# Kernel tuning notes

Measured on AMD Instinct MI355X. Metric: run time of the kernel, lower is better.

The kernel has to match this reference:

```python
import jax, jax.numpy as jnp
from jax import lax
import numpy as np

CLASS_NUMBER = 19
REGION_RADIUS = 1
KERNEL = 2 * REGION_RADIUS + 1  # 3
IMAGE_TOPK = 256
EPS = 1e-6


def setup_inputs() -> dict:
    key = jax.random.key(0)
    # softmax-like probabilities over classes
    raw = jax.random.uniform(key, (4, CLASS_NUMBER, 512, 1024), dtype=jnp.float32)
    logit = raw / jnp.sum(raw, axis=1, keepdims=True)
    return {"logit": logit}


def _box_sum(x):
    # kxk box sum with zero padding (SAME for odd kernel == pad=radius)
    return lax.reduce_window(x, jnp.float32(0), lax.add,
                             (1, 1, KERNEL, KERNEL), (1, 1, 1, 1), 'SAME')


def reference(logit):
    B, C, H, W = logit.shape
    logC = jnp.log(jnp.float32(C))

    # region uncertainty: normalized entropy, then avg-pool (count_include_pad)
    entropy = jnp.sum(-logit * jnp.log(logit + EPS), axis=1, keepdims=True) / logC
    region_uncertainty = _box_sum(entropy) / (KERNEL * KERNEL)  # [B,1,H,W]

    # region impurity: argmax -> one-hot -> depthwise box-sum (ones kernel)
    predict = jnp.argmax(logit, axis=1)                       # [B,H,W]
    one_hot = jax.nn.one_hot(predict, C, axis=1, dtype=logit.dtype)  # [B,C,H,W]
    summary = _box_sum(one_hot)                               # [B,C,H,W]
    count = jnp.sum(summary, axis=1, keepdims=True)           # [B,1,H,W]
    dist = summary / count
    region_impurity = jnp.sum(-dist * jnp.log(dist + EPS), axis=1, keepdims=True) / logC

    score = region_uncertainty * region_impurity              # [B,1,H,W]

    # per-image score: sum of top-k region scores
    flat = score.reshape(B, H * W)
    topk_vals, _ = lax.top_k(flat, IMAGE_TOPK)
    image_score = jnp.sum(topk_vals, axis=1)                  # [B]
    return image_score
```

## Files before the change

kernel.cpp:

```cpp
#include <hip/hip_runtime.h>
#include <cstdint>
#include <cstddef>

#define BB 4
#define CC 19
#define HH 512
#define WW 1024
#define HW (HH*WW)
#define HW4 (HW/4)
#define BHW (BB*HW)
#define KTOP 256
#define EPSF 1e-6f
#define NB1 4096
#define NB2 8192
#define SEG 128
#define LSTRIDE 1032
#define LOGC 2.9444389791664403f

__device__ __forceinline__ unsigned int sortable(float x) {
    unsigned int u = __float_as_uint(x);
    return (u & 0x80000000u) ? ~u : (u | 0x80000000u);
}
__device__ __forceinline__ float unsortable(unsigned int K) {
    unsigned int u = (K & 0x80000000u) ? (K & 0x7FFFFFFFu) : ~K;
    return __uint_as_float(u);
}

__global__ __launch_bounds__(256) void k_ent(const float4* __restrict__ logit,
                                             float4* __restrict__ ent,
                                             uchar4* __restrict__ pred,
                                             unsigned int* __restrict__ histz,
                                             float* __restrict__ outz) {
    int idx = blockIdx.x * 256 + threadIdx.x;
    if (idx < 81928) histz[idx] = 0;
    if (idx < BB) outz[idx] = 0.f;
    int b = idx >> 17;
    int q = idx & (HW4 - 1);
    const float4* base = logit + (size_t)b * CC * HW4 + q;
    float e0 = 0.f, e1 = 0.f, e2 = 0.f, e3 = 0.f;
    float m0 = -1.f, m1 = -1.f, m2 = -1.f, m3 = -1.f;
    int a0 = 0, a1 = 0, a2 = 0, a3 = 0;
#pragma unroll
    for (int c = 0; c < CC; ++c) {
        float4 p = base[(size_t)c * HW4];
        e0 -= p.x * __logf(p.x + EPSF); if (p.x > m0) { m0 = p.x; a0 = c; }
        e1 -= p.y * __logf(p.y + EPSF); if (p.y > m1) { m1 = p.y; a1 = c; }
        e2 -= p.z * __logf(p.z + EPSF); if (p.z > m2) { m2 = p.z; a2 = c; }
        e3 -= p.w * __logf(p.w + EPSF); if (p.w > m3) { m3 = p.w; a3 = c; }
    }
    ent[idx] = make_float4(e0, e1, e2, e3);
    pred[idx] = make_uchar4((unsigned char)a0, (unsigned char)a1,
                            (unsigned char)a2, (unsigned char)a3);
}

__global__ __launch_bounds__(256) void k_score_hist(const float* __restrict__ ent,
                                                    const unsigned char* __restrict__ pred,
                                                    float* __restrict__ score,
                                                    unsigned int* __restrict__ hist1) {
    __shared__ __align__(16) float ent_s[6 * LSTRIDE];
    __shared__ __align__(16) unsigned char pred_s[6 * LSTRIDE];
    __shared__ unsigned int lh[NB1];
    __shared__ float lgt[48];
    int tid = threadIdx.x;
    int b = blockIdx.x >> 7;
    int seg = blockIdx.x & (SEG - 1);
    int r0 = seg * 4;

    for (int i = tid; i < 6 * LSTRIDE; i += 256) { ent_s[i] = 0.f; pred_s[i] = 255; }
    for (int i = tid; i < NB1; i += 256) lh[i] = 0;
    if (tid < 48) {
        int nvi = tid >> 4, cnt = tid & 15;
        float nv = (nvi == 0) ? 4.f : (nvi == 1) ? 6.f : 9.f;
        lgt[tid] = __logf((float)cnt / nv + EPSF);
    }
    __syncthreads();

    const float* eb = ent + (size_t)b * HW;
    const unsigned char* pb = pred + (size_t)b * HW;
    for (int i = tid; i < 1536; i += 256) {
        int rr = i >> 8, c4 = i & 255;
        int g = r0 - 1 + rr;
        if (g >= 0 && g < HH) {
            float4 v = *(const float4*)(eb + g * WW + c4 * 4);
            *(float4*)&ent_s[rr * LSTRIDE + 4 + c4 * 4] = v;
            uchar4 pv = *(const uchar4*)(pb + g * WW + c4 * 4);
            *(uchar4*)&pred_s[rr * LSTRIDE + 4 + c4 * 4] = pv;
        }
    }
    __syncthreads();

    float* sbuf = score + (size_t)b * HW;
#pragma unroll
    for (int it = 0; it < 16; ++it) {
        int p = it * 256 + tid;
        int py = p >> 10, px = p & 1023;
        int h = r0 + py, w = px;
        int l0 = py * LSTRIDE + 3 + px;
        float es = 0.f;
        int cls[9];
#pragma unroll
        for (int i = 0; i < 9; ++i) {
            int o = l0 + (i / 3) * LSTRIDE + (i % 3);
            es += ent_s[o];
            cls[i] = pred_s[o];
        }
        int nv = ((h > 0) + (h < HH - 1) + 1) * ((w > 0) + (w < WW - 1) + 1);
        float inv = 1.f / (float)nv;
        int nvi = (nv == 9) ? 2 : ((nv == 6) ? 1 : 0);
        const float* lg = &lgt[nvi * 16];
        float lsum = 0.f;
#pragma unroll
        for (int i = 0; i < 9; ++i) {
            int cnt = 0;
#pragma unroll
            for (int j = 0; j < 9; ++j) cnt += (cls[j] == cls[i]) ? 1 : 0;
            float lv = lg[cnt];
            lsum += (cls[i] != 255) ? lv : 0.f;
        }
        float imp = -inv * lsum;
        float v = (es * (1.f / (9.f * LOGC))) * (imp * (1.f / LOGC));
        sbuf[h * WW + w] = v;
        atomicAdd(&lh[sortable(v) >> 20], 1u);
    }
    __syncthreads();
    unsigned int* hb = hist1 + (size_t)b * NB1;
    for (int i = tid; i < NB1; i += 256) {
        unsigned int c = lh[i];
        if (c) atomicAdd(&hb[i], c);
    }
}

__device__ __forceinline__ void select4k(const unsigned int* __restrict__ hb,
                                         int rem, int* bin_out, int* rem_out) {
    __shared__ unsigned int cs[256];
    __shared__ unsigned int bs[16];
    __shared__ int s_chunk, s_bin, s_rem;
    int t = threadIdx.x;
    unsigned int s = 0;
#pragma unroll
    for (int i = 0; i < 16; ++i) s += hb[t * 16 + i];
    cs[t] = s;
    __syncthreads();
    for (int d = 1; d < 256; d <<= 1) {
        unsigned int v = (t + d < 256) ? cs[t + d] : 0;
        __syncthreads();
        cs[t] += v;
        __syncthreads();
    }
    unsigned int St = cs[t];
    unsigned int St1 = (t < 255) ? cs[t + 1] : 0;
    if ((int)St >= rem && (t == 255 || (int)St1 < rem)) {
        s_chunk = t; s_rem = rem - (int)St1;
    }
    __syncthreads();
    int chunk = s_chunk, rem2 = s_rem;
    if (t < 16) bs[t] = hb[chunk * 16 + t];
    __syncthreads();
    for (int d = 1; d < 16; d <<= 1) {
        unsigned int v = (t < 16 && t + d < 16) ? bs[t + d] : 0;
        __syncthreads();
        if (t < 16) bs[t] += v;
        __syncthreads();
    }
    if (t < 16) {
        unsigned int Sb = bs[t];
        unsigned int Sb1 = (t < 15) ? bs[t + 1] : 0;
        if ((int)Sb >= rem2 && (t == 15 || (int)Sb1 < rem2)) {
            s_bin = chunk * 16 + t; s_rem = rem2 - (int)Sb1;
        }
    }
    __syncthreads();
    *bin_out = s_bin;
    *rem_out = s_rem;
}

__device__ __forceinline__ void select8k(const unsigned int* __restrict__ hb,
                                         int rem, int* bin_out, int* rem_out) {
    __shared__ unsigned int cs[256];
    __shared__ unsigned int bs[32];
    __shared__ int s_chunk, s_bin, s_rem;
    int t = threadIdx.x;
    unsigned int s = 0;
#pragma unroll 8
    for (int i = 0; i < 32; ++i) s += hb[t * 32 + i];
    cs[t] = s;
    __syncthreads();
    for (int d = 1; d < 256; d <<= 1) {
        unsigned int v = (t + d < 256) ? cs[t + d] : 0;
        __syncthreads();
        cs[t] += v;
        __syncthreads();
    }
    unsigned int St = cs[t];
    unsigned int St1 = (t < 255) ? cs[t + 1] : 0;
    if ((int)St >= rem && (t == 255 || (int)St1 < rem)) {
        s_chunk = t; s_rem = rem - (int)St1;
    }
    __syncthreads();
    int chunk = s_chunk, rem2 = s_rem;
    if (t < 32) bs[t] = hb[chunk * 32 + t];
    __syncthreads();
    for (int d = 1; d < 32; d <<= 1) {
        unsigned int v = (t < 32 && t + d < 32) ? bs[t + d] : 0;
        __syncthreads();
        if (t < 32) bs[t] += v;
        __syncthreads();
    }
    if (t < 32) {
        unsigned int Sb = bs[t];
        unsigned int Sb1 = (t < 31) ? bs[t + 1] : 0;
        if ((int)Sb >= rem2 && (t == 31 || (int)Sb1 < rem2)) {
            s_bin = chunk * 32 + t; s_rem = rem2 - (int)Sb1;
        }
    }
    __syncthreads();
    *bin_out = s_bin;
    *rem_out = s_rem;
}

__global__ __launch_bounds__(256) void k_hist2(const float4* __restrict__ score,
                                               const unsigned int* __restrict__ hist1,
                                               unsigned int* __restrict__ hist2,
                                               float* __restrict__ hsum,
                                               unsigned int* __restrict__ T1g,
                                               int* __restrict__ r1g,
                                               float* __restrict__ out) {
    __shared__ unsigned int lh[NB2];
    __shared__ float ls[NB2];
    __shared__ float red[4];
    int b = blockIdx.x >> 7;
    int seg = blockIdx.x & (SEG - 1);
    int bin1, rem1;
    select4k(hist1 + (size_t)b * NB1, KTOP, &bin1, &rem1);
    unsigned int t1 = (unsigned int)bin1;
    if (seg == 0 && threadIdx.x == 0) { T1g[b] = t1; r1g[b] = rem1; }
    for (int i = threadIdx.x; i < NB2; i += 256) { lh[i] = 0; ls[i] = 0.f; }
    __syncthreads();
    const float4* p = score + ((size_t)b * HW + (size_t)seg * (HW / SEG)) / 4;
    float sa = 0.f;
    for (int i = threadIdx.x; i < (HW / SEG) / 4; i += 256) {
        float4 v = p[i];
        float vv[4] = {v.x, v.y, v.z, v.w};
#pragma unroll
        for (int q = 0; q < 4; ++q) {
            unsigned int k = sortable(vv[q]);
            unsigned int cb = k >> 20;
            if (cb > t1) sa += vv[q];
            else if (cb == t1) {
                int sub = (k >> 7) & 0x1FFF;
                atomicAdd(&lh[sub], 1u);
                atomicAdd(&ls[sub], vv[q]);
            }
        }
    }
    __syncthreads();
    unsigned int* hb = hist2 + (size_t)b * NB2;
    float* sb = hsum + (size_t)b * NB2;
    for (int i = threadIdx.x; i < NB2; i += 256) {
        unsigned int c = lh[i];
        if (c) { atomicAdd(&hb[i], c); atomicAdd(&sb[i], ls[i]); }
    }
#pragma unroll
    for (int d = 32; d; d >>= 1) sa += __shfl_down(sa, d);
    if ((threadIdx.x & 63) == 0) red[threadIdx.x >> 6] = sa;
    __syncthreads();
    if (threadIdx.x == 0) {
        float tt = red[0] + red[1] + red[2] + red[3];
        if (tt != 0.f) atomicAdd(&out[b], tt);
    }
}

__global__ __launch_bounds__(256) void k_scan2(const unsigned int* __restrict__ hist2,
                                               const float* __restrict__ hsum,
                                               const unsigned int* __restrict__ T1g,
                                               const int* __restrict__ r1g,
                                               float* __restrict__ out) {
    int b = blockIdx.x;
    int bin, rem;
    select8k(hist2 + (size_t)b * NB2, r1g[b], &bin, &rem);
    __shared__ float rs[256];
    int t = threadIdx.x;
    const float* sb = hsum + (size_t)b * NB2;
    float s = 0.f;
    for (int i = t; i < NB2; i += 256) if (i > bin) s += sb[i];
    rs[t] = s;
    __syncthreads();
    for (int d = 128; d; d >>= 1) {
        if (t < d) rs[t] += rs[t + d];
        __syncthreads();
    }
    if (t == 0) {
        unsigned int K = (T1g[b] << 20) | ((unsigned int)bin << 7);
        out[b] += rs[0] + unsortable(K) * (float)rem;
    }
}

extern "C" void kernel_launch(void* const* d_in, const int* in_sizes, int n_in,
                              void* d_out, int out_size, void* d_ws, size_t ws_size,
                              hipStream_t stream) {
    const float* logit = (const float*)d_in[0];
    float* out = (float*)d_out;
    char* ws = (char*)d_ws;

    float*         ent   = (float*)(ws);
    unsigned char* pred  = (unsigned char*)(ws + 8388608);
    float*         score = (float*)(ws + 10485760);
    unsigned int*  histb = (unsigned int*)(ws + 18874368);
    unsigned int*  hist1 = histb;
    unsigned int*  hist2 = histb + 16384;
    float*         hsum  = (float*)(histb + 49152);
    unsigned int*  T1g   = histb + 81920;
    int*           r1g   = (int*)(histb + 81924);

    k_ent<<<BHW / 4 / 256, 256, 0, stream>>>((const float4*)logit, (float4*)ent,
                                             (uchar4*)pred, histb, out);
    k_score_hist<<<BB * SEG, 256, 0, stream>>>(ent, pred, score, hist1);
    k_hist2<<<BB * SEG, 256, 0, stream>>>((const float4*)score, hist1,
                                          hist2, hsum, T1g, r1g, out);
    k_scan2<<<BB, 256, 0, stream>>>(hist2, hsum, T1g, r1g, out);
}
```

Baseline: 289.9 us.

## Fuse all stages into one cooperative persistent kernel with grid syncs

Replaces the four-kernel pipeline with a single cooperative kernel of 256 blocks. Each block computes entropy and argmax for 8 rows straight into shared memory and exchanges only the halo rows through global memory. Scores stay in registers for the second histogram pass, so the score buffer is never written or reread. The aim is to remove launch gaps and the intermediate ent, pred and score traffic. The cost is three grid-wide barriers, only 256 blocks of parallelism for the bandwidth-heavy logit read, and a fallback to the old path if the cooperative launch fails.

```diff
diff --git a/kernel.cpp b/kernel.cpp
--- a/kernel.cpp
+++ b/kernel.cpp
@@ -1,6 +1,9 @@
 #include <hip/hip_runtime.h>
+#include <hip/hip_cooperative_groups.h>
 #include <cstdint>
 #include <cstddef>
+
+namespace cg = cooperative_groups;
 
 #define BB 4
 #define CC 19
@@ -13,9 +16,12 @@
 #define EPSF 1e-6f
 #define NB1 4096
 #define NB2 8192
-#define SEG 128
 #define LSTRIDE 1032
 #define LOGC 2.9444389791664403f
+
+#define NSEG 64
+#define RPB 8
+#define SEGF 128
 
 __device__ __forceinline__ unsigned int sortable(float x) {
     unsigned int u = __float_as_uint(x);
@@ -24,6 +30,314 @@
 __device__ __forceinline__ float unsortable(unsigned int K) {
     unsigned int u = (K & 0x80000000u) ? (K & 0x7FFFFFFFu) : ~K;
     return __uint_as_float(u);
+}
+__device__ __forceinline__ unsigned int agld(const unsigned int* p) {
+    return __hip_atomic_load(p, __ATOMIC_RELAXED, __HIP_MEMORY_SCOPE_AGENT);
+}
+__device__ __forceinline__ void agst(unsigned int* p, unsigned int v) {
+    __hip_atomic_store(p, v, __ATOMIC_RELAXED, __HIP_MEMORY_SCOPE_AGENT);
+}
+
+struct P1Mem8 {
+    float ent_s[(RPB + 2) * LSTRIDE];
+    unsigned char pred_s[(RPB + 2) * LSTRIDE];
+    unsigned int lh1[NB1];
+};
+struct P2Mem8 {
+    unsigned int lh2[NB2];
+    float ls2[NB2];
+};
+union UMem8 { P1Mem8 p1; P2Mem8 p2; };
+
+__device__ __forceinline__ void sel_coarse(const unsigned int* __restrict__ hb,
+                                           int rem, unsigned int* cs, unsigned int* bs,
+                                           int* s3, int* bin_out, int* rem_out) {
+    int t = threadIdx.x;
+    unsigned int s = 0;
+#pragma unroll
+    for (int i = 0; i < 16; ++i) s += agld(&hb[t * 16 + i]);
+    cs[t] = s;
+    __syncthreads();
+    for (int d = 1; d < 256; d <<= 1) {
+        unsigned int v = (t + d < 256) ? cs[t + d] : 0;
+        __syncthreads();
+        cs[t] += v;
+        __syncthreads();
+    }
+    unsigned int St = cs[t];
+    unsigned int St1 = (t < 255) ? cs[t + 1] : 0;
+    if ((int)St >= rem && (t == 255 || (int)St1 < rem)) {
+        s3[0] = t; s3[2] = rem - (int)St1;
+    }
+    __syncthreads();
+    int chunk = s3[0], rem2 = s3[2];
+    if (t < 16) bs[t] = agld(&hb[chunk * 16 + t]);
+    __syncthreads();
+    for (int d = 1; d < 16; d <<= 1) {
+        unsigned int v = (t < 16 && t + d < 16) ? bs[t + d] : 0;
+        __syncthreads();
+        if (t < 16) bs[t] += v;
+        __syncthreads();
+    }
+    if (t < 16) {
+        unsigned int Sb = bs[t];
+        unsigned int Sb1 = (t < 15) ? bs[t + 1] : 0;
+        if ((int)Sb >= rem2 && (t == 15 || (int)Sb1 < rem2)) {
+            s3[1] = chunk * 16 + t; s3[2] = rem2 - (int)Sb1;
+        }
+    }
+    __syncthreads();
+    *bin_out = s3[1];
+    *rem_out = s3[2];
+}
+
+__device__ __forceinline__ void sel_fine(const unsigned int* __restrict__ hb,
+                                         int rem, unsigned int* cs, unsigned int* bs,
+                                         int* s3, int* bin_out, int* rem_out) {
+    int t = threadIdx.x;
+    unsigned int s = 0;
+#pragma unroll 8
+    for (int i = 0; i < 32; ++i) s += agld(&hb[t * 32 + i]);
+    cs[t] = s;
+    __syncthreads();
+    for (int d = 1; d < 256; d <<= 1) {
+        unsigned int v = (t + d < 256) ? cs[t + d] : 0;
+        __syncthreads();
+        cs[t] += v;
+        __syncthreads();
+    }
+    unsigned int St = cs[t];
+    unsigned int St1 = (t < 255) ? cs[t + 1] : 0;
+    if ((int)St >= rem && (t == 255 || (int)St1 < rem)) {
+        s3[0] = t; s3[2] = rem - (int)St1;
+    }
+    __syncthreads();
+    int chunk = s3[0], rem2 = s3[2];
+    if (t < 32) bs[t] = agld(&hb[chunk * 32 + t]);
+    __syncthreads();
+    for (int d = 1; d < 32; d <<= 1) {
+        unsigned int v = (t < 32 && t + d < 32) ? bs[t + d] : 0;
+        __syncthreads();
+        if (t < 32) bs[t] += v;
+        __syncthreads();
+    }
+    if (t < 32) {
+        unsigned int Sb = bs[t];
+        unsigned int Sb1 = (t < 31) ? bs[t + 1] : 0;
+        if ((int)Sb >= rem2 && (t == 31 || (int)Sb1 < rem2)) {
+            s3[1] = chunk * 32 + t; s3[2] = rem2 - (int)Sb1;
+        }
+    }
+    __syncthreads();
+    *bin_out = s3[1];
+    *rem_out = s3[2];
+}
+
+__global__ __launch_bounds__(256, 2) void k_fused8(const float* __restrict__ logit,
+                                                   float* __restrict__ ent,
+                                                   unsigned char* __restrict__ pred,
+                                                   unsigned int* __restrict__ histb,
+                                                   float* __restrict__ out) {
+    __shared__ __align__(16) UMem8 U;
+    __shared__ float lgt[48];
+    __shared__ unsigned int cs[256];
+    __shared__ unsigned int bs[32];
+    __shared__ int s3[3];
+    __shared__ float red[4];
+    __shared__ float rs[256];
+
+    cg::grid_group grid = cg::this_grid();
+    int tid = threadIdx.x;
+    int b = blockIdx.x >> 6;
+    int seg = blockIdx.x & (NSEG - 1);
+    int r0 = seg * RPB;
+
+    unsigned int* hist1 = histb;
+    unsigned int* hist2 = histb + 16384;
+    float*        hsum  = (float*)(histb + 49152);
+
+    int gid = blockIdx.x * 256 + tid;
+    for (int i = gid; i < 81920; i += 256 * 256) agst(&histb[i], 0u);
+    if (gid < BB) agst((unsigned int*)&out[gid], 0u);
+    if (tid < 48) {
+        int nvi = tid >> 4, cnt = tid & 15;
+        float nv = (nvi == 0) ? 4.f : (nvi == 1) ? 6.f : 9.f;
+        lgt[tid] = __logf((float)cnt / nv + EPSF);
+    }
+    for (int i = tid; i < (RPB + 2) * LSTRIDE; i += 256) { U.p1.ent_s[i] = 0.f; U.p1.pred_s[i] = 255; }
+    for (int i = tid; i < NB1; i += 256) U.p1.lh1[i] = 0;
+    __syncthreads();
+
+    {
+        const float4* bb4 = (const float4*)logit + (size_t)b * CC * HW4;
+        int q0 = r0 * 256;
+#pragma unroll
+        for (int it = 0; it < RPB; ++it) {
+            int q = q0 + it * 256 + tid;
+            const float4* basep = bb4 + q;
+            float e0 = 0.f, e1 = 0.f, e2 = 0.f, e3 = 0.f;
+            float m0 = -1.f, m1 = -1.f, m2 = -1.f, m3 = -1.f;
+            int a0 = 0, a1 = 0, a2 = 0, a3 = 0;
+#pragma unroll
+            for (int c = 0; c < CC; ++c) {
+                float4 p = basep[(size_t)c * HW4];
+                e0 -= p.x * __logf(p.x + EPSF); if (p.x > m0) { m0 = p.x; a0 = c; }
+                e1 -= p.y * __logf(p.y + EPSF); if (p.y > m1) { m1 = p.y; a1 = c; }
+                e2 -= p.z * __logf(p.z + EPSF); if (p.z > m2) { m2 = p.z; a2 = c; }
+                e3 -= p.w * __logf(p.w + EPSF); if (p.w > m3) { m3 = p.w; a3 = c; }
+            }
+            *(float4*)&U.p1.ent_s[(it + 1) * LSTRIDE + 4 + tid * 4] = make_float4(e0, e1, e2, e3);
+            U.p1.pred_s[(it + 1) * LSTRIDE + 4 + tid * 4 + 0] = (unsigned char)a0;
+            U.p1.pred_s[(it + 1) * LSTRIDE + 4 + tid * 4 + 1] = (unsigned char)a1;
+            U.p1.pred_s[(it + 1) * LSTRIDE + 4 + tid * 4 + 2] = (unsigned char)a2;
+            U.p1.pred_s[(it + 1) * LSTRIDE + 4 + tid * 4 + 3] = (unsigned char)a3;
+            if (it == 0 || it == RPB - 1) {
+                unsigned int* ep = (unsigned int*)ent + ((size_t)b * HW4 + q) * 4;
+                agst(ep + 0, __float_as_uint(e0));
+                agst(ep + 1, __float_as_uint(e1));
+                agst(ep + 2, __float_as_uint(e2));
+                agst(ep + 3, __float_as_uint(e3));
+                unsigned int pw = (unsigned int)a0 | ((unsigned int)a1 << 8) |
+                                  ((unsigned int)a2 << 16) | ((unsigned int)a3 << 24);
+                agst((unsigned int*)pred + (size_t)b * HW4 + q, pw);
+            }
+        }
+    }
+    grid.sync();
+
+    for (int i = tid; i < 512; i += 256) {
+        int top = i >> 8;
+        int rr = top * (RPB + 1);
+        int c4 = i & 255;
+        int g = r0 - 1 + top * (RPB + 1);
+        if (g >= 0 && g < HH) {
+            const unsigned int* es4 = (const unsigned int*)ent + ((size_t)b * HW4 + (size_t)g * 256 + c4) * 4;
+            float4 v;
+            v.x = __uint_as_float(agld(es4 + 0));
+            v.y = __uint_as_float(agld(es4 + 1));
+            v.z = __uint_as_float(agld(es4 + 2));
+            v.w = __uint_as_float(agld(es4 + 3));
+            *(float4*)&U.p1.ent_s[rr * LSTRIDE + 4 + c4 * 4] = v;
+            unsigned int pw = agld((const unsigned int*)pred + (size_t)b * HW4 + (size_t)g * 256 + c4);
+            *(unsigned int*)&U.p1.pred_s[rr * LSTRIDE + 4 + c4 * 4] = pw;
+        }
+    }
+    __syncthreads();
+
+    float sv[4 * RPB];
+#pragma unroll
+    for (int k = 0; k < RPB; ++k) {
+        float r3[3][6];
+        int p3[3][6];
+#pragma unroll
+        for (int rr = 0; rr < 3; ++rr) {
+            const float* rowp = &U.p1.ent_s[(k + rr) * LSTRIDE + 4];
+            const unsigned char* prow = &U.p1.pred_s[(k + rr) * LSTRIDE + 4];
+            float4 m = *(const float4*)&rowp[tid * 4];
+            r3[rr][0] = rowp[tid * 4 - 1];
+            r3[rr][1] = m.x; r3[rr][2] = m.y; r3[rr][3] = m.z; r3[rr][4] = m.w;
+            r3[rr][5] = rowp[tid * 4 + 4];
+            uchar4 pm = *(const uchar4*)&prow[tid * 4];
+            p3[rr][0] = prow[tid * 4 - 1];
+            p3[rr][1] = pm.x; p3[rr][2] = pm.y; p3[rr][3] = pm.z; p3[rr][4] = pm.w;
+            p3[rr][5] = prow[tid * 4 + 4];
+        }
+        int h = r0 + k;
+        int hn = (h > 0) + (h < HH - 1) + 1;
+#pragma unroll
+        for (int q = 0; q < 4; ++q) {
+            int w = tid * 4 + q;
+            float es = 0.f;
+#pragma unroll
+            for (int i = 0; i < 9; ++i) es += r3[i / 3][q + i % 3];
+            int cls[9];
+#pragma unroll
+            for (int i = 0; i < 9; ++i) cls[i] = p3[i / 3][q + i % 3];
+            int nv = hn * ((w > 0) + (w < WW - 1) + 1);
+            float inv = 1.f / (float)nv;
+            int nvi = (nv == 9) ? 2 : ((nv == 6) ? 1 : 0);
+            const float* lg = &lgt[nvi * 16];
+            float lsum = 0.f;
+#pragma unroll
+            for (int i = 0; i < 9; ++i) {
+                int cnt = 0;
+#pragma unroll
+                for (int j = 0; j < 9; ++j) cnt += (cls[j] == cls[i]) ? 1 : 0;
+                float lv = lg[cnt];
+                lsum += (cls[i] != 255) ? lv : 0.f;
+            }
+            float imp = -inv * lsum;
+            float v = (es * (1.f / (9.f * LOGC))) * (imp * (1.f / LOGC));
+            sv[k * 4 + q] = v;
+            atomicAdd(&U.p1.lh1[sortable(v) >> 20], 1u);
+        }
+    }
+    __syncthreads();
+    {
+        unsigned int* hb = hist1 + (size_t)b * NB1;
+        for (int i = tid; i < NB1; i += 256) {
+            unsigned int c = U.p1.lh1[i];
+            if (c) atomicAdd(&hb[i], c);
+        }
+    }
+    grid.sync();
+
+    int bin1, rem1;
+    sel_coarse(hist1 + (size_t)b * NB1, KTOP, cs, bs, s3, &bin1, &rem1);
+    unsigned int t1 = (unsigned int)bin1;
+    for (int i = tid; i < NB2; i += 256) { U.p2.lh2[i] = 0; U.p2.ls2[i] = 0.f; }
+    __syncthreads();
+    float sa = 0.f;
+#pragma unroll
+    for (int j = 0; j < 4 * RPB; ++j) {
+        float vv = sv[j];
+        unsigned int k = sortable(vv);
+        unsigned int cb = k >> 20;
+        if (cb > t1) sa += vv;
+        else if (cb == t1) {
+            int sub = (k >> 7) & 0x1FFF;
+            atomicAdd(&U.p2.lh2[sub], 1u);
+            atomicAdd(&U.p2.ls2[sub], vv);
+        }
+    }
+    __syncthreads();
+    {
+        unsigned int* hb = hist2 + (size_t)b * NB2;
+        float* sb = hsum + (size_t)b * NB2;
+        for (int i = tid; i < NB2; i += 256) {
+            unsigned int c = U.p2.lh2[i];
+            if (c) { atomicAdd(&hb[i], c); atomicAdd(&sb[i], U.p2.ls2[i]); }
+        }
+    }
+#pragma unroll
+    for (int d = 32; d; d >>= 1) sa += __shfl_down(sa, d);
+    if ((tid & 63) == 0) red[tid >> 6] = sa;
+    __syncthreads();
+    if (tid == 0) {
+        float tt = red[0] + red[1] + red[2] + red[3];
+        if (tt != 0.f) atomicAdd(&out[b], tt);
+    }
+    grid.sync();
+
+    if (seg == 0) {
+        int bin, rem;
+        sel_fine(hist2 + (size_t)b * NB2, rem1, cs, bs, s3, &bin, &rem);
+        const float* sb = hsum + (size_t)b * NB2;
+        float s = 0.f;
+        for (int i = tid; i < NB2; i += 256)
+            if (i > bin) s += __uint_as_float(agld((const unsigned int*)&sb[i]));
+        rs[tid] = s;
+        __syncthreads();
+        for (int d = 128; d; d >>= 1) {
+            if (tid < d) rs[tid] += rs[tid + d];
+            __syncthreads();
+        }
+        if (tid == 0) {
+            unsigned int K = (t1 << 20) | ((unsigned int)bin << 7);
+            float cur = __uint_as_float(agld((const unsigned int*)&out[b]));
+            agst((unsigned int*)&out[b], __float_as_uint(cur + rs[0] + unsortable(K) * (float)rem));
+        }
+    }
 }
 
 __global__ __launch_bounds__(256) void k_ent(const float4* __restrict__ logit,
@@ -63,7 +377,7 @@
     __shared__ float lgt[48];
     int tid = threadIdx.x;
     int b = blockIdx.x >> 7;
-    int seg = blockIdx.x & (SEG - 1);
+    int seg = blockIdx.x & (SEGF - 1);
     int r0 = seg * 4;
 
     for (int i = tid; i < 6 * LSTRIDE; i += 256) { ent_s[i] = 0.f; pred_s[i] = 255; }
@@ -229,16 +543,16 @@
     __shared__ float ls[NB2];
     __shared__ float red[4];
     int b = blockIdx.x >> 7;
-    int seg = blockIdx.x & (SEG - 1);
+    int seg = blockIdx.x & (SEGF - 1);
     int bin1, rem1;
     select4k(hist1 + (size_t)b * NB1, KTOP, &bin1, &rem1);
     unsigned int t1 = (unsigned int)bin1;
     if (seg == 0 && threadIdx.x == 0) { T1g[b] = t1; r1g[b] = rem1; }
     for (int i = threadIdx.x; i < NB2; i += 256) { lh[i] = 0; ls[i] = 0.f; }
     __syncthreads();
-    const float4* p = score + ((size_t)b * HW + (size_t)seg * (HW / SEG)) / 4;
+    const float4* p = score + ((size_t)b * HW + (size_t)seg * (HW / SEGF)) / 4;
     float sa = 0.f;
-    for (int i = threadIdx.x; i < (HW / SEG) / 4; i += 256) {
+    for (int i = threadIdx.x; i < (HW / SEGF) / 4; i += 256) {
         float4 v = p[i];
         float vv[4] = {v.x, v.y, v.z, v.w};
 #pragma unroll
@@ -312,10 +626,16 @@
     unsigned int*  T1g   = histb + 81920;
     int*           r1g   = (int*)(histb + 81924);
 
-    k_ent<<<BHW / 4 / 256, 256, 0, stream>>>((const float4*)logit, (float4*)ent,
-                                             (uchar4*)pred, histb, out);
-    k_score_hist<<<BB * SEG, 256, 0, stream>>>(ent, pred, score, hist1);
-    k_hist2<<<BB * SEG, 256, 0, stream>>>((const float4*)score, hist1,
-                                          hist2, hsum, T1g, r1g, out);
-    k_scan2<<<BB, 256, 0, stream>>>(hist2, hsum, T1g, r1g, out);
-}
+    void* args[] = { (void*)&logit, (void*)&ent, (void*)&pred, (void*)&histb, (void*)&out };
+    hipError_t err = hipLaunchCooperativeKernel(k_fused8, dim3(BB * NSEG), dim3(256),
+                                                args, 0u, stream);
+    if (err != hipSuccess) {
+        (void)hipGetLastError();
+        k_ent<<<BHW / 4 / 256, 256, 0, stream>>>((const float4*)logit, (float4*)ent,
+                                                 (uchar4*)pred, histb, out);
+        k_score_hist<<<BB * SEGF, 256, 0, stream>>>(ent, pred, score, hist1);
+        k_hist2<<<BB * SEGF, 256, 0, stream>>>((const float4*)score, hist1,
+                                               hist2, hsum, T1g, r1g, out);
+        k_scan2<<<BB, 256, 0, stream>>>(hist2, hsum, T1g, r1g, out);
+    }
+}
```

Result: slower. 374.6 us (+29.2%).

## Fuse entropy, score, and two-pass top-k into one persistent kernel with grid barriers

Applied to the files above, without the earlier changes.

Replaces the four-kernel pipeline with an init kernel plus one persistent kernel of 256 blocks of 1024 threads, separated by software grid barriers. Each block computes entropy and argmax for its 8-row strip directly into shared memory and writes only the boundary rows to global for halo exchange. Scores stay in registers for the second histogram pass, so the full score map is never written or re-read. It relies on all 256 blocks being co-resident for the spin barrier, and it exposes less parallelism while streaming the large logit input.

```diff
diff --git a/kernel.cpp b/kernel.cpp
--- a/kernel.cpp
+++ b/kernel.cpp
@@ -8,14 +8,17 @@
 #define WW 1024
 #define HW (HH*WW)
 #define HW4 (HW/4)
-#define BHW (BB*HW)
 #define KTOP 256
 #define EPSF 1e-6f
 #define NB1 4096
 #define NB2 8192
-#define SEG 128
 #define LSTRIDE 1032
 #define LOGC 2.9444389791664403f
+
+#define NSEG 64
+#define RPB 8
+#define NBLK (BB*NSEG)
+#define TPB 1024
 
 __device__ __forceinline__ unsigned int sortable(float x) {
     unsigned int u = __float_as_uint(x);
@@ -26,272 +29,274 @@
     return __uint_as_float(u);
 }
 
-__global__ __launch_bounds__(256) void k_ent(const float4* __restrict__ logit,
-                                             float4* __restrict__ ent,
-                                             uchar4* __restrict__ pred,
-                                             unsigned int* __restrict__ histz,
-                                             float* __restrict__ outz) {
-    int idx = blockIdx.x * 256 + threadIdx.x;
-    if (idx < 81928) histz[idx] = 0;
-    if (idx < BB) outz[idx] = 0.f;
-    int b = idx >> 17;
-    int q = idx & (HW4 - 1);
-    const float4* base = logit + (size_t)b * CC * HW4 + q;
-    float e0 = 0.f, e1 = 0.f, e2 = 0.f, e3 = 0.f;
-    float m0 = -1.f, m1 = -1.f, m2 = -1.f, m3 = -1.f;
-    int a0 = 0, a1 = 0, a2 = 0, a3 = 0;
-#pragma unroll
-    for (int c = 0; c < CC; ++c) {
-        float4 p = base[(size_t)c * HW4];
-        e0 -= p.x * __logf(p.x + EPSF); if (p.x > m0) { m0 = p.x; a0 = c; }
-        e1 -= p.y * __logf(p.y + EPSF); if (p.y > m1) { m1 = p.y; a1 = c; }
-        e2 -= p.z * __logf(p.z + EPSF); if (p.z > m2) { m2 = p.z; a2 = c; }
-        e3 -= p.w * __logf(p.w + EPSF); if (p.w > m3) { m3 = p.w; a3 = c; }
-    }
-    ent[idx] = make_float4(e0, e1, e2, e3);
-    pred[idx] = make_uchar4((unsigned char)a0, (unsigned char)a1,
-                            (unsigned char)a2, (unsigned char)a3);
-}
-
-__global__ __launch_bounds__(256) void k_score_hist(const float* __restrict__ ent,
-                                                    const unsigned char* __restrict__ pred,
-                                                    float* __restrict__ score,
-                                                    unsigned int* __restrict__ hist1) {
-    __shared__ __align__(16) float ent_s[6 * LSTRIDE];
-    __shared__ __align__(16) unsigned char pred_s[6 * LSTRIDE];
-    __shared__ unsigned int lh[NB1];
+__device__ __forceinline__ void gbar(unsigned int* cnt, unsigned int* gen) {
+    __threadfence();
+    __syncthreads();
+    if (threadIdx.x == 0) {
+        unsigned int g = __hip_atomic_load(gen, __ATOMIC_RELAXED, __HIP_MEMORY_SCOPE_AGENT);
+        unsigned int a = __hip_atomic_fetch_add(cnt, 1u, __ATOMIC_ACQ_REL, __HIP_MEMORY_SCOPE_AGENT);
+        if (a == NBLK - 1u) {
+            __hip_atomic_store(cnt, 0u, __ATOMIC_RELAXED, __HIP_MEMORY_SCOPE_AGENT);
+            __hip_atomic_fetch_add(gen, 1u, __ATOMIC_RELEASE, __HIP_MEMORY_SCOPE_AGENT);
+        } else {
+            while (__hip_atomic_load(gen, __ATOMIC_ACQUIRE, __HIP_MEMORY_SCOPE_AGENT) == g)
+                __builtin_amdgcn_s_sleep(16);
+        }
+    }
+    __syncthreads();
+    __threadfence();
+}
+
+struct P1Mem {
+    float ent_s[(RPB + 2) * LSTRIDE];
+    unsigned char pred_s[(RPB + 2) * LSTRIDE];
+    unsigned int lh1[NB1];
+};
+struct P2Mem {
+    unsigned int lh2[NB2];
+    float ls2[NB2];
+};
+union UMem { P1Mem p1; P2Mem p2; };
+
+template<int CPT>
+__device__ __forceinline__ void sel_topdown(const unsigned int* __restrict__ hb,
+                                            int rem, unsigned int* cs, unsigned int* bs,
+                                            int* s3, int* bin_out, int* rem_out) {
+    int t = threadIdx.x;
+    unsigned int s = 0;
+#pragma unroll
+    for (int i = 0; i < CPT; ++i) s += hb[t * CPT + i];
+    cs[t] = s;
+    __syncthreads();
+    for (int d = 1; d < 1024; d <<= 1) {
+        unsigned int v = (t + d < 1024) ? cs[t + d] : 0;
+        __syncthreads();
+        cs[t] += v;
+        __syncthreads();
+    }
+    unsigned int St = cs[t];
+    unsigned int St1 = (t < 1023) ? cs[t + 1] : 0;
+    if ((int)St >= rem && (t == 1023 || (int)St1 < rem)) {
+        s3[0] = t; s3[2] = rem - (int)St1;
+    }
+    __syncthreads();
+    int chunk = s3[0], rem2 = s3[2];
+    if (t < CPT) bs[t] = hb[chunk * CPT + t];
+    __syncthreads();
+    if (t == 0) {
+        int acc = 0, bin = chunk * CPT, rr = rem2;
+        for (int j = CPT - 1; j >= 0; --j) {
+            acc += (int)bs[j];
+            if (acc >= rem2) { bin = chunk * CPT + j; rr = rem2 - (acc - (int)bs[j]); break; }
+        }
+        s3[1] = bin; s3[2] = rr;
+    }
+    __syncthreads();
+    *bin_out = s3[1];
+    *rem_out = s3[2];
+}
+
+__global__ __launch_bounds__(1024) void k_init(unsigned int* __restrict__ histb,
+                                               float* __restrict__ out) {
+    int i = blockIdx.x * 1024 + threadIdx.x;
+    if (i < 81922) histb[i] = 0u;
+    if (i < BB) out[i] = 0.f;
+}
+
+__global__ __launch_bounds__(1024) void k_fused(const float* __restrict__ logit,
+                                                float* __restrict__ ent,
+                                                unsigned char* __restrict__ pred,
+                                                unsigned int* __restrict__ histb,
+                                                float* __restrict__ out) {
+    __shared__ __align__(16) UMem U;
     __shared__ float lgt[48];
+    __shared__ unsigned int cs[1024];
+    __shared__ unsigned int bs[8];
+    __shared__ int s3[3];
+    __shared__ float red[16];
+
     int tid = threadIdx.x;
-    int b = blockIdx.x >> 7;
-    int seg = blockIdx.x & (SEG - 1);
-    int r0 = seg * 4;
-
-    for (int i = tid; i < 6 * LSTRIDE; i += 256) { ent_s[i] = 0.f; pred_s[i] = 255; }
-    for (int i = tid; i < NB1; i += 256) lh[i] = 0;
+    int tx = tid & 255;
+    int ty = tid >> 8;
+    int b = blockIdx.x >> 6;
+    int seg = blockIdx.x & (NSEG - 1);
+    int r0 = seg * RPB;
+
+    unsigned int* hist1 = histb;
+    unsigned int* hist2 = histb + 16384;
+    float*        hsum  = (float*)(histb + 49152);
+    unsigned int* bcnt  = histb + 81920;
+    unsigned int* bgen  = histb + 81921;
+
     if (tid < 48) {
         int nvi = tid >> 4, cnt = tid & 15;
         float nv = (nvi == 0) ? 4.f : (nvi == 1) ? 6.f : 9.f;
         lgt[tid] = __logf((float)cnt / nv + EPSF);
     }
-    __syncthreads();
-
-    const float* eb = ent + (size_t)b * HW;
-    const unsigned char* pb = pred + (size_t)b * HW;
-    for (int i = tid; i < 1536; i += 256) {
-        int rr = i >> 8, c4 = i & 255;
-        int g = r0 - 1 + rr;
+    for (int i = tid; i < (RPB + 2) * LSTRIDE; i += TPB) { U.p1.ent_s[i] = 0.f; U.p1.pred_s[i] = 255; }
+    for (int i = tid; i < NB1; i += TPB) U.p1.lh1[i] = 0;
+    __syncthreads();
+
+    {
+        const float4* bb4 = (const float4*)logit + (size_t)b * CC * HW4;
+#pragma unroll
+        for (int it = 0; it < 2; ++it) {
+            int lr = ty + it * 4;
+            int q = (r0 + lr) * 256 + tx;
+            const float4* basep = bb4 + q;
+            float e0 = 0.f, e1 = 0.f, e2 = 0.f, e3 = 0.f;
+            float m0 = -1.f, m1 = -1.f, m2 = -1.f, m3 = -1.f;
+            int a0 = 0, a1 = 0, a2 = 0, a3 = 0;
+#pragma unroll
+            for (int c = 0; c < CC; ++c) {
+                float4 p = basep[(size_t)c * HW4];
+                e0 -= p.x * __logf(p.x + EPSF); if (p.x > m0) { m0 = p.x; a0 = c; }
+                e1 -= p.y * __logf(p.y + EPSF); if (p.y > m1) { m1 = p.y; a1 = c; }
+                e2 -= p.z * __logf(p.z + EPSF); if (p.z > m2) { m2 = p.z; a2 = c; }
+                e3 -= p.w * __logf(p.w + EPSF); if (p.w > m3) { m3 = p.w; a3 = c; }
+            }
+            float4 ev = make_float4(e0, e1, e2, e3);
+            unsigned int pw = (unsigned int)a0 | ((unsigned int)a1 << 8) |
+                              ((unsigned int)a2 << 16) | ((unsigned int)a3 << 24);
+            *(float4*)&U.p1.ent_s[(lr + 1) * LSTRIDE + 4 + tx * 4] = ev;
+            *(unsigned int*)&U.p1.pred_s[(lr + 1) * LSTRIDE + 4 + tx * 4] = pw;
+            if (lr == 0 || lr == RPB - 1) {
+                *((float4*)ent + (size_t)b * HW4 + q) = ev;
+                ((unsigned int*)pred)[(size_t)b * HW4 + q] = pw;
+            }
+        }
+    }
+    gbar(bcnt, bgen);
+
+    if (tid < 512) {
+        int top = tid >> 8;
+        int c4 = tid & 255;
+        int rr = top * (RPB + 1);
+        int g = r0 - 1 + top * (RPB + 1);
         if (g >= 0 && g < HH) {
-            float4 v = *(const float4*)(eb + g * WW + c4 * 4);
-            *(float4*)&ent_s[rr * LSTRIDE + 4 + c4 * 4] = v;
-            uchar4 pv = *(const uchar4*)(pb + g * WW + c4 * 4);
-            *(uchar4*)&pred_s[rr * LSTRIDE + 4 + c4 * 4] = pv;
-        }
-    }
-    __syncthreads();
-
-    float* sbuf = score + (size_t)b * HW;
-#pragma unroll
-    for (int it = 0; it < 16; ++it) {
-        int p = it * 256 + tid;
-        int py = p >> 10, px = p & 1023;
-        int h = r0 + py, w = px;
-        int l0 = py * LSTRIDE + 3 + px;
-        float es = 0.f;
-        int cls[9];
-#pragma unroll
-        for (int i = 0; i < 9; ++i) {
-            int o = l0 + (i / 3) * LSTRIDE + (i % 3);
-            es += ent_s[o];
-            cls[i] = pred_s[o];
-        }
-        int nv = ((h > 0) + (h < HH - 1) + 1) * ((w > 0) + (w < WW - 1) + 1);
-        float inv = 1.f / (float)nv;
-        int nvi = (nv == 9) ? 2 : ((nv == 6) ? 1 : 0);
-        const float* lg = &lgt[nvi * 16];
-        float lsum = 0.f;
-#pragma unroll
-        for (int i = 0; i < 9; ++i) {
-            int cnt = 0;
-#pragma unroll
-            for (int j = 0; j < 9; ++j) cnt += (cls[j] == cls[i]) ? 1 : 0;
-            float lv = lg[cnt];
-            lsum += (cls[i] != 255) ? lv : 0.f;
-        }
-        float imp = -inv * lsum;
-        float v = (es * (1.f / (9.f * LOGC))) * (imp * (1.f / LOGC));
-        sbuf[h * WW + w] = v;
-        atomicAdd(&lh[sortable(v) >> 20], 1u);
-    }
-    __syncthreads();
-    unsigned int* hb = hist1 + (size_t)b * NB1;
-    for (int i = tid; i < NB1; i += 256) {
-        unsigned int c = lh[i];
-        if (c) atomicAdd(&hb[i], c);
-    }
-}
-
-__device__ __forceinline__ void select4k(const unsigned int* __restrict__ hb,
-                                         int rem, int* bin_out, int* rem_out) {
-    __shared__ unsigned int cs[256];
-    __shared__ unsigned int bs[16];
-    __shared__ int s_chunk, s_bin, s_rem;
-    int t = threadIdx.x;
-    unsigned int s = 0;
-#pragma unroll
-    for (int i = 0; i < 16; ++i) s += hb[t * 16 + i];
-    cs[t] = s;
-    __syncthreads();
-    for (int d = 1; d < 256; d <<= 1) {
-        unsigned int v = (t + d < 256) ? cs[t + d] : 0;
+            float4 v = *((const float4*)ent + (size_t)b * HW4 + (size_t)g * 256 + c4);
+            *(float4*)&U.p1.ent_s[rr * LSTRIDE + 4 + c4 * 4] = v;
+            unsigned int pw = ((const unsigned int*)pred)[(size_t)b * HW4 + (size_t)g * 256 + c4];
+            *(unsigned int*)&U.p1.pred_s[rr * LSTRIDE + 4 + c4 * 4] = pw;
+        }
+    }
+    __syncthreads();
+
+    float sv[8];
+#pragma unroll
+    for (int it = 0; it < 2; ++it) {
+        int k = ty + it * 4;
+        float r3[3][6];
+        int p3[3][6];
+#pragma unroll
+        for (int rr = 0; rr < 3; ++rr) {
+            const float* rowp = &U.p1.ent_s[(k + rr) * LSTRIDE + 4];
+            const unsigned char* prow = &U.p1.pred_s[(k + rr) * LSTRIDE + 4];
+            float4 m = *(const float4*)&rowp[tx * 4];
+            r3[rr][0] = rowp[tx * 4 - 1];
+            r3[rr][1] = m.x; r3[rr][2] = m.y; r3[rr][3] = m.z; r3[rr][4] = m.w;
+            r3[rr][5] = rowp[tx * 4 + 4];
+            uchar4 pm = *(const uchar4*)&prow[tx * 4];
+            p3[rr][0] = prow[tx * 4 - 1];
+            p3[rr][1] = pm.x; p3[rr][2] = pm.y; p3[rr][3] = pm.z; p3[rr][4] = pm.w;
+            p3[rr][5] = prow[tx * 4 + 4];
+        }
+        int h = r0 + k;
+        int hn = (h > 0) + (h < HH - 1) + 1;
+#pragma unroll
+        for (int q = 0; q < 4; ++q) {
+            int w = tx * 4 + q;
+            float es = 0.f;
+#pragma unroll
+            for (int i = 0; i < 9; ++i) es += r3[i / 3][q + i % 3];
+            int cls[9];
+#pragma unroll
+            for (int i = 0; i < 9; ++i) cls[i] = p3[i / 3][q + i % 3];
+            int nv = hn * ((w > 0) + (w < WW - 1) + 1);
+            float inv = 1.f / (float)nv;
+            int nvi = (nv == 9) ? 2 : ((nv == 6) ? 1 : 0);
+            const float* lg = &lgt[nvi * 16];
+            float lsum = 0.f;
+#pragma unroll
+            for (int i = 0; i < 9; ++i) {
+                int cnt = 0;
+#pragma unroll
+                for (int j = 0; j < 9; ++j) cnt += (cls[j] == cls[i]) ? 1 : 0;
+                float lv = lg[cnt];
+                lsum += (cls[i] != 255) ? lv : 0.f;
+            }
+            float imp = -inv * lsum;
+            float v = (es * (1.f / (9.f * LOGC))) * (imp * (1.f / LOGC));
+            sv[it * 4 + q] = v;
+            atomicAdd(&U.p1.lh1[sortable(v) >> 20], 1u);
+        }
+    }
+    __syncthreads();
+    {
+        unsigned int* hb = hist1 + (size_t)b * NB1;
+        for (int i = tid; i < NB1; i += TPB) {
+            unsigned int c = U.p1.lh1[i];
+            if (c) atomicAdd(&hb[i], c);
+        }
+    }
+    gbar(bcnt, bgen);
+
+    int bin1, rem1;
+    sel_topdown<4>(hist1 + (size_t)b * NB1, KTOP, cs, bs, s3, &bin1, &rem1);
+    unsigned int t1 = (unsigned int)bin1;
+    for (int i = tid; i < NB2; i += TPB) { U.p2.lh2[i] = 0; U.p2.ls2[i] = 0.f; }
+    __syncthreads();
+    float sa = 0.f;
+#pragma unroll
+    for (int j = 0; j < 8; ++j) {
+        float vv = sv[j];
+        unsigned int k = sortable(vv);
+        unsigned int cb = k >> 20;
+        if (cb > t1) sa += vv;
+        else if (cb == t1) {
+            int sub = (k >> 7) & 0x1FFF;
+            atomicAdd(&U.p2.lh2[sub], 1u);
+            atomicAdd(&U.p2.ls2[sub], vv);
+        }
+    }
+    __syncthreads();
+    {
+        unsigned int* hb = hist2 + (size_t)b * NB2;
+        float* sb = hsum + (size_t)b * NB2;
+        for (int i = tid; i < NB2; i += TPB) {
+            unsigned int c = U.p2.lh2[i];
+            if (c) { atomicAdd(&hb[i], c); atomicAdd(&sb[i], U.p2.ls2[i]); }
+        }
+    }
+#pragma unroll
+    for (int d = 32; d; d >>= 1) sa += __shfl_down(sa, d);
+    if ((tid & 63) == 0) red[tid >> 6] = sa;
+    __syncthreads();
+    if (tid == 0) {
+        float tt = 0.f;
+#pragma unroll
+        for (int i = 0; i < 16; ++i) tt += red[i];
+        if (tt != 0.f) atomicAdd(&out[b], tt);
+    }
+    gbar(bcnt, bgen);
+
+    if (seg == 0) {
+        int bin, rem;
+        sel_topdown<8>(hist2 + (size_t)b * NB2, rem1, cs, bs, s3, &bin, &rem);
+        const float* sb = hsum + (size_t)b * NB2;
+        float* rsf = (float*)cs;
+        float s = 0.f;
+        for (int i = tid; i < NB2; i += TPB) if (i > bin) s += sb[i];
+        rsf[tid] = s;
         __syncthreads();
-        cs[t] += v;
-        __syncthreads();
-    }
-    unsigned int St = cs[t];
-    unsigned int St1 = (t < 255) ? cs[t + 1] : 0;
-    if ((int)St >= rem && (t == 255 || (int)St1 < rem)) {
-        s_chunk = t; s_rem = rem - (int)St1;
-    }
-    __syncthreads();
-    int chunk = s_chunk, rem2 = s_rem;
-    if (t < 16) bs[t] = hb[chunk * 16 + t];
-    __syncthreads();
-    for (int d = 1; d < 16; d <<= 1) {
-        unsigned int v = (t < 16 && t + d < 16) ? bs[t + d] : 0;
-        __syncthreads();
-        if (t < 16) bs[t] += v;
-        __syncthreads();
-    }
-    if (t < 16) {
-        unsigned int Sb = bs[t];
-        unsigned int Sb1 = (t < 15) ? bs[t + 1] : 0;
-        if ((int)Sb >= rem2 && (t == 15 || (int)Sb1 < rem2)) {
-            s_bin = chunk * 16 + t; s_rem = rem2 - (int)Sb1;
-        }
-    }
-    __syncthreads();
-    *bin_out = s_bin;
-    *rem_out = s_rem;
-}
-
-__device__ __forceinline__ void select8k(const unsigned int* __restrict__ hb,
-                                         int rem, int* bin_out, int* rem_out) {
-    __shared__ unsigned int cs[256];
-    __shared__ unsigned int bs[32];
-    __shared__ int s_chunk, s_bin, s_rem;
-    int t = threadIdx.x;
-    unsigned int s = 0;
-#pragma unroll 8
-    for (int i = 0; i < 32; ++i) s += hb[t * 32 + i];
-    cs[t] = s;
-    __syncthreads();
-    for (int d = 1; d < 256; d <<= 1) {
-        unsigned int v = (t + d < 256) ? cs[t + d] : 0;
-        __syncthreads();
-        cs[t] += v;
-        __syncthreads();
-    }
-    unsigned int St = cs[t];
-    unsigned int St1 = (t < 255) ? cs[t + 1] : 0;
-    if ((int)St >= rem && (t == 255 || (int)St1 < rem)) {
-        s_chunk = t; s_rem = rem - (int)St1;
-    }
-    __syncthreads();
-    int chunk = s_chunk, rem2 = s_rem;
-    if (t < 32) bs[t] = hb[chunk * 32 + t];
-    __syncthreads();
-    for (int d = 1; d < 32; d <<= 1) {
-        unsigned int v = (t < 32 && t + d < 32) ? bs[t + d] : 0;
-        __syncthreads();
-        if (t < 32) bs[t] += v;
-        __syncthreads();
-    }
-    if (t < 32) {
-        unsigned int Sb = bs[t];
-        unsigned int Sb1 = (t < 31) ? bs[t + 1] : 0;
-        if ((int)Sb >= rem2 && (t == 31 || (int)Sb1 < rem2)) {
-            s_bin = chunk * 32 + t; s_rem = rem2 - (int)Sb1;
-        }
-    }
-    __syncthreads();
-    *bin_out = s_bin;
-    *rem_out = s_rem;
-}
-
-__global__ __launch_bounds__(256) void k_hist2(const float4* __restrict__ score,
-                                               const unsigned int* __restrict__ hist1,
-                                               unsigned int* __restrict__ hist2,
-                                               float* __restrict__ hsum,
-                                               unsigned int* __restrict__ T1g,
-                                               int* __restrict__ r1g,
-                                               float* __restrict__ out) {
-    __shared__ unsigned int lh[NB2];
-    __shared__ float ls[NB2];
-    __shared__ float red[4];
-    int b = blockIdx.x >> 7;
-    int seg = blockIdx.x & (SEG - 1);
-    int bin1, rem1;
-    select4k(hist1 + (size_t)b * NB1, KTOP, &bin1, &rem1);
-    unsigned int t1 = (unsigned int)bin1;
-    if (seg == 0 && threadIdx.x == 0) { T1g[b] = t1; r1g[b] = rem1; }
-    for (int i = threadIdx.x; i < NB2; i += 256) { lh[i] = 0; ls[i] = 0.f; }
-    __syncthreads();
-    const float4* p = score + ((size_t)b * HW + (size_t)seg * (HW / SEG)) / 4;
-    float sa = 0.f;
-    for (int i = threadIdx.x; i < (HW / SEG) / 4; i += 256) {
-        float4 v = p[i];
-        float vv[4] = {v.x, v.y, v.z, v.w};
-#pragma unroll
-        for (int q = 0; q < 4; ++q) {
-            unsigned int k = sortable(vv[q]);
-            unsigned int cb = k >> 20;
-            if (cb > t1) sa += vv[q];
-            else if (cb == t1) {
-                int sub = (k >> 7) & 0x1FFF;
-                atomicAdd(&lh[sub], 1u);
-                atomicAdd(&ls[sub], vv[q]);
-            }
-        }
-    }
-    __syncthreads();
-    unsigned int* hb = hist2 + (size_t)b * NB2;
-    float* sb = hsum + (size_t)b * NB2;
-    for (int i = threadIdx.x; i < NB2; i += 256) {
-        unsigned int c = lh[i];
-        if (c) { atomicAdd(&hb[i], c); atomicAdd(&sb[i], ls[i]); }
-    }
-#pragma unroll
-    for (int d = 32; d; d >>= 1) sa += __shfl_down(sa, d);
-    if ((threadIdx.x & 63) == 0) red[threadIdx.x >> 6] = sa;
-    __syncthreads();
-    if (threadIdx.x == 0) {
-        float tt = red[0] + red[1] + red[2] + red[3];
-        if (tt != 0.f) atomicAdd(&out[b], tt);
-    }
-}
-
-__global__ __launch_bounds__(256) void k_scan2(const unsigned int* __restrict__ hist2,
-                                               const float* __restrict__ hsum,
-                                               const unsigned int* __restrict__ T1g,
-                                               const int* __restrict__ r1g,
-                                               float* __restrict__ out) {
-    int b = blockIdx.x;
-    int bin, rem;
-    select8k(hist2 + (size_t)b * NB2, r1g[b], &bin, &rem);
-    __shared__ float rs[256];
-    int t = threadIdx.x;
-    const float* sb = hsum + (size_t)b * NB2;
-    float s = 0.f;
-    for (int i = t; i < NB2; i += 256) if (i > bin) s += sb[i];
-    rs[t] = s;
-    __syncthreads();
-    for (int d = 128; d; d >>= 1) {
-        if (t < d) rs[t] += rs[t + d];
-        __syncthreads();
-    }
-    if (t == 0) {
-        unsigned int K = (T1g[b] << 20) | ((unsigned int)bin << 7);
-        out[b] += rs[0] + unsortable(K) * (float)rem;
+        for (int d = 512; d; d >>= 1) {
+            if (tid < d) rsf[tid] += rsf[tid + d];
+            __syncthreads();
+        }
+        if (tid == 0) {
+            unsigned int K = (t1 << 20) | ((unsigned int)bin << 7);
+            atomicAdd(&out[b], rsf[0] + unsortable(K) * (float)rem);
+        }
     }
 }
 
@@ -304,18 +309,8 @@
 
     float*         ent   = (float*)(ws);
     unsigned char* pred  = (unsigned char*)(ws + 8388608);
-    float*         score = (float*)(ws + 10485760);
-    unsigned int*  histb = (unsigned int*)(ws + 18874368);
-    unsigned int*  hist1 = histb;
-    unsigned int*  hist2 = histb + 16384;
-    float*         hsum  = (float*)(histb + 49152);
-    unsigned int*  T1g   = histb + 81920;
-    int*           r1g   = (int*)(histb + 81924);
-
-    k_ent<<<BHW / 4 / 256, 256, 0, stream>>>((const float4*)logit, (float4*)ent,
-                                             (uchar4*)pred, histb, out);
-    k_score_hist<<<BB * SEG, 256, 0, stream>>>(ent, pred, score, hist1);
-    k_hist2<<<BB * SEG, 256, 0, stream>>>((const float4*)score, hist1,
-                                          hist2, hsum, T1g, r1g, out);
-    k_scan2<<<BB, 256, 0, stream>>>(hist2, hsum, T1g, r1g, out);
-}
+    unsigned int*  histb = (unsigned int*)(ws + 10485760);
+
+    k_init<<<81, 1024, 0, stream>>>(histb, out);
+    k_fused<<<NBLK, TPB, 0, stream>>>(logit, ent, pred, histb, out);
+}
```

Result: slower. 731.3 us (+152.2%).
